# Kernel optimization log

Hardware: AMD Instinct MI355X
Metric: run time of the kernel (lower is better)

The kernel has to match this reference:

```python
import jax, jax.numpy as jnp
from jax import lax
import numpy as np

KPAD = 2  # padding for 5x5 kernel, 'same' output

def setup_inputs() -> dict:
    key = jax.random.key(0)
    x = jax.random.normal(key, (16, 8, 512, 512), dtype=jnp.float32)
    # fixed 5x5 averaging kernel, matching torch.ones(5,5)/25
    weight = jnp.ones((1, 1, 5, 5), dtype=jnp.float32) / 25.0
    return {"x": x, "weight": weight}

def reference(x, weight):
    # Per-channel (depthwise) 5x5 box blur. The torch code loops conv2d over
    # split channels; a single grouped conv with feature_group_count=C is the
    # same math in one fused op.
    C = x.shape[1]
    k = jnp.tile(weight, (C, 1, 1, 1))  # (C,1,5,5) OIHW with groups=C
    return lax.conv_general_dilated(
        x, k,
        window_strides=(1, 1),
        padding=[(KPAD, KPAD), (KPAD, KPAD)],
        dimension_numbers=("NCHW", "OIHW", "NCHW"),
        feature_group_count=C,
    )
```

## Files before the change

### kernel.cpp

```cpp
#include <hip/hip_runtime.h>


#define H 512
#define W 512
#define TH 16
#define TW 256
#define LROWS (TH + 4)
#define LCOLS (TW + 8)
#define NV (LCOLS / 4)

__global__ __launch_bounds__(256) void avefilter_kernel(
    const float* __restrict__ x, const float* __restrict__ wgt,
    float* __restrict__ out)
{
    __shared__ float smem[LROWS * LCOLS];

    const int tid   = threadIdx.x;
    const int bx    = blockIdx.x;
    const int rt    = bx >> 1;
    const int ct    = bx & 1;
    const int plane = blockIdx.y;

    const int r0  = rt * TH;
    const int gc0 = ct * TW;

    const float* in   = x   + (size_t)plane * (H * W);
    float*       outp = out + (size_t)plane * (H * W);
    const float scale = wgt[0];

    for (int i = tid; i < LROWS * NV; i += 256) {
        const int lr = i / NV;
        const int lv = i - lr * NV;
        const int gr = r0 - 2 + lr;
        const int gc = gc0 - 4 + lv * 4;
        float4 v = make_float4(0.f, 0.f, 0.f, 0.f);
        if (gr >= 0 && gr < H && gc >= 0 && gc < W) {
            v = *(const float4*)(in + (size_t)gr * W + gc);
        }
        *(float4*)(smem + lr * LCOLS + lv * 4) = v;
    }
    __syncthreads();

    const float* bcol = smem + tid + 2;

    float h[5];
    #pragma unroll
    for (int i = 0; i < 5; ++i) {
        const float* b = bcol + i * LCOLS;
        h[i] = b[0] + b[1] + b[2] + b[3] + b[4];
    }

    #pragma unroll
    for (int r = 0; r < TH; ++r) {
        float s = h[0] + h[1] + h[2] + h[3] + h[4];
        outp[(size_t)(r0 + r) * W + gc0 + tid] = s * scale;
        if (r < TH - 1) {
            const float* b = bcol + (r + 5) * LCOLS;
            h[r % 5] = b[0] + b[1] + b[2] + b[3] + b[4];
        }
    }
}

extern "C" void kernel_launch(void* const* d_in, const int* in_sizes, int n_in,
                              void* d_out, int out_size, void* d_ws, size_t ws_size,
                              hipStream_t stream) {
    const float* x   = (const float*)d_in[0];
    const float* wgt = (const float*)d_in[1];
    float* out = (float*)d_out;

    dim3 grid((H / TH) * 2, 16 * 8);
    dim3 block(256);
    avefilter_kernel<<<grid, block, 0, stream>>>(x, wgt, out);
}
```

Before: 235.0 us.

## Replace shared-memory tiling with register sliding window over full-width rows

Drops the shared-memory tile and barrier. Each thread now owns four adjacent columns across the full 512-wide row and loads each input row straight from global memory as a float2+float4+float2 triple. It keeps a 5-row ring of horizontal partial sums in registers and stores float4 outputs. Border handling moves from zero-filled smem to clamped row indices with multiplicative masks. Halo rows are still re-read between the two 16-row groups, and register pressure rises.

```diff
diff --git a/kernel.cpp b/kernel.cpp
--- a/kernel.cpp
+++ b/kernel.cpp
@@ -3,61 +3,93 @@
 
 #define H 512
 #define W 512
-#define TH 16
-#define TW 256
-#define LROWS (TH + 4)
-#define LCOLS (TW + 8)
-#define NV (LCOLS / 4)
+#define RB 32
+#define GR 16
+
+struct RowV { float2 l; float4 m; float2 r; };
+
+__device__ __forceinline__ RowV load_row(const float* __restrict__ in, int rr,
+                                         int offL, int c0, int offR) {
+    const int rc = rr < 0 ? 0 : (rr > (H - 1) ? (H - 1) : rr);
+    const float* p = in + (size_t)rc * W;
+    RowV v;
+    v.l = *reinterpret_cast<const float2*>(p + offL);
+    v.m = *reinterpret_cast<const float4*>(p + c0);
+    v.r = *reinterpret_cast<const float2*>(p + offR);
+    return v;
+}
+
+__device__ __forceinline__ void hsum4(const RowV& v, float mrow, float mL, float mR,
+                                      float& s0, float& s1, float& s2, float& s3) {
+    const float a0 = v.l.x * mL, a1 = v.l.y * mL;
+    const float b4 = v.r.x * mR, b5 = v.r.y * mR;
+    const float t1 = v.m.x + v.m.y;
+    const float t2 = v.m.z + v.m.w;
+    s0 = (a0 + a1 + t1 + v.m.z) * mrow;
+    s1 = (a1 + t1 + t2) * mrow;
+    s2 = (t1 + t2 + b4) * mrow;
+    s3 = (v.m.y + t2 + b4 + b5) * mrow;
+}
 
 __global__ __launch_bounds__(256) void avefilter_kernel(
     const float* __restrict__ x, const float* __restrict__ wgt,
     float* __restrict__ out)
 {
-    __shared__ float smem[LROWS * LCOLS];
+    const int t     = threadIdx.x;
+    const int g     = t >> 7;
+    const int lt    = t & 127;
+    const int c0    = lt << 2;
+    const int plane = blockIdx.y;
+    const int r0    = blockIdx.x * RB + g * GR;
 
-    const int tid   = threadIdx.x;
-    const int bx    = blockIdx.x;
-    const int rt    = bx >> 1;
-    const int ct    = bx & 1;
-    const int plane = blockIdx.y;
-
-    const int r0  = rt * TH;
-    const int gc0 = ct * TW;
-
-    const float* in   = x   + (size_t)plane * (H * W);
-    float*       outp = out + (size_t)plane * (H * W);
+    const float* in = x + (size_t)plane * (H * W);
+    float* op = out + (size_t)plane * (H * W) + (size_t)r0 * W + c0;
     const float scale = wgt[0];
 
-    for (int i = tid; i < LROWS * NV; i += 256) {
-        const int lr = i / NV;
-        const int lv = i - lr * NV;
-        const int gr = r0 - 2 + lr;
-        const int gc = gc0 - 4 + lv * 4;
-        float4 v = make_float4(0.f, 0.f, 0.f, 0.f);
-        if (gr >= 0 && gr < H && gc >= 0 && gc < W) {
-            v = *(const float4*)(in + (size_t)gr * W + gc);
-        }
-        *(float4*)(smem + lr * LCOLS + lv * 4) = v;
-    }
-    __syncthreads();
+    const float mL = (lt != 0)   ? 1.f : 0.f;
+    const float mR = (lt != 127) ? 1.f : 0.f;
+    const int  offL = (lt != 0)   ? (c0 - 2) : c0;
+    const int  offR = (lt != 127) ? (c0 + 4) : c0;
 
-    const float* bcol = smem + tid + 2;
+    float h[4][5];
 
-    float h[5];
-    #pragma unroll
-    for (int i = 0; i < 5; ++i) {
-        const float* b = bcol + i * LCOLS;
-        h[i] = b[0] + b[1] + b[2] + b[3] + b[4];
-    }
+    RowV p0  = load_row(in, r0 - 2, offL, c0, offR);
+    RowV p1  = load_row(in, r0 - 1, offL, c0, offR);
+    RowV p2  = load_row(in, r0,     offL, c0, offR);
+    RowV p3  = load_row(in, r0 + 1, offL, c0, offR);
+    RowV cur = load_row(in, r0 + 2, offL, c0, offR);
+
+    const float mtop = (r0 == 0) ? 0.f : 1.f;
+    hsum4(p0, mtop, mL, mR, h[0][0], h[1][0], h[2][0], h[3][0]);
+    hsum4(p1, mtop, mL, mR, h[0][1], h[1][1], h[2][1], h[3][1]);
+    hsum4(p2, 1.f,  mL, mR, h[0][2], h[1][2], h[2][2], h[3][2]);
+    hsum4(p3, 1.f,  mL, mR, h[0][3], h[1][3], h[2][3], h[3][3]);
 
     #pragma unroll
-    for (int r = 0; r < TH; ++r) {
-        float s = h[0] + h[1] + h[2] + h[3] + h[4];
-        outp[(size_t)(r0 + r) * W + gc0 + tid] = s * scale;
-        if (r < TH - 1) {
-            const float* b = bcol + (r + 5) * LCOLS;
-            h[r % 5] = b[0] + b[1] + b[2] + b[3] + b[4];
-        }
+    for (int i = 0; i < GR - 1; ++i) {
+        RowV nxt = load_row(in, r0 + 3 + i, offL, c0, offR);
+        const int   s    = (i + 4) % 5;
+        const float mrow = ((unsigned)(r0 + 2 + i) < (unsigned)H) ? 1.f : 0.f;
+        hsum4(cur, mrow, mL, mR, h[0][s], h[1][s], h[2][s], h[3][s]);
+        float4 o;
+        o.x = (h[0][0] + h[0][1] + h[0][2] + h[0][3] + h[0][4]) * scale;
+        o.y = (h[1][0] + h[1][1] + h[1][2] + h[1][3] + h[1][4]) * scale;
+        o.z = (h[2][0] + h[2][1] + h[2][2] + h[2][3] + h[2][4]) * scale;
+        o.w = (h[3][0] + h[3][1] + h[3][2] + h[3][3] + h[3][4]) * scale;
+        *reinterpret_cast<float4*>(op + (size_t)i * W) = o;
+        cur = nxt;
+    }
+    {
+        const int   i    = GR - 1;
+        const int   s    = (i + 4) % 5;
+        const float mrow = ((unsigned)(r0 + 2 + i) < (unsigned)H) ? 1.f : 0.f;
+        hsum4(cur, mrow, mL, mR, h[0][s], h[1][s], h[2][s], h[3][s]);
+        float4 o;
+        o.x = (h[0][0] + h[0][1] + h[0][2] + h[0][3] + h[0][4]) * scale;
+        o.y = (h[1][0] + h[1][1] + h[1][2] + h[1][3] + h[1][4]) * scale;
+        o.z = (h[2][0] + h[2][1] + h[2][2] + h[2][3] + h[2][4]) * scale;
+        o.w = (h[3][0] + h[3][1] + h[3][2] + h[3][3] + h[3][4]) * scale;
+        *reinterpret_cast<float4*>(op + (size_t)i * W) = o;
     }
 }
 
@@ -68,7 +100,7 @@
     const float* wgt = (const float*)d_in[1];
     float* out = (float*)d_out;
 
-    dim3 grid((H / TH) * 2, 16 * 8);
+    dim3 grid(H / RB, 16 * 8);
     dim3 block(256);
     avefilter_kernel<<<grid, block, 0, stream>>>(x, wgt, out);
 }
```

Measured after the change: 231.7 us. Within noise of the previous version (-1.4%).
